# Optimization experiments

Hardware: AMD Instinct MI355X
Metric: run time of the kernel (lower is better)

Reference implementation:

```python
import jax, jax.numpy as jnp
import jax.scipy as jsp
import numpy as np

NUM_EMBEDDINGS = 256
EMBEDDING_DIM = 64
SPARSITY_LEVEL = 4
N_BINS = 16
COEF_MAX = 3.0
COEF_MU = 50.0
COMMITMENT_COST = 0.25
EPSILON = 1e-10


def _normalize_dict(dictionary):
    # F.normalize(dict, p=2, dim=0, eps): x / max(||x||_2, eps) per column
    nrm = jnp.linalg.norm(dictionary, axis=0, keepdims=True)
    return dictionary / jnp.maximum(nrm, EPSILON)


def _quantize_coeff_mu_law(coeff):
    inv_log1p_mu = 1.0 / np.log1p(COEF_MU)  # scalar constant
    c = jnp.clip(coeff, -COEF_MAX, COEF_MAX) / COEF_MAX
    encoded = jnp.sign(c) * jnp.log1p(jnp.abs(c) * COEF_MU) * inv_log1p_mu
    scaled = (encoded + 1.0) * ((N_BINS - 1) / 2.0)
    bin_idx = jnp.clip(jnp.round(scaled).astype(jnp.int32), 0, N_BINS - 1)
    # dequantize
    z = bin_idx.astype(coeff.dtype) * (2.0 / (N_BINS - 1)) - 1.0
    decoded = jnp.sign(z) * (jnp.expm1(jnp.abs(z) / inv_log1p_mu) / COEF_MU) * COEF_MAX
    return bin_idx, decoded


def batch_omp_with_support(X, Dn, K):
    # X: [M, Bs] signals, Dn: [M, N] normalized dictionary
    G = Dn.T @ Dn                       # [N, N] Gram
    h_bar = (Dn.T @ X).T                # [Bs, N] correlations
    Bs, N = h_bar.shape
    dt = h_bar.dtype
    h = h_bar
    mask = jnp.zeros((Bs, N), dtype=bool)
    L = jnp.ones((Bs, 1, 1), dtype=dt)  # incremental Cholesky of G[I, I]
    I = jnp.zeros((Bs, 0), dtype=jnp.int32)
    x_sel = jnp.zeros((Bs, 0), dtype=dt)
    rows = jnp.arange(Bs)
    for k in range(1, K + 1):  # K is small & static -> unrolled
        idx = jnp.argmax(jnp.abs(h) * (~mask), axis=1).astype(jnp.int32)
        mask = mask.at[rows, idx].set(True)
        if k > 1:
            G_stack = G[I, idx[:, None]]                     # [Bs, k-1]
            w = jsp.linalg.solve_triangular(L, G_stack[..., None], lower=True)  # [Bs,k-1,1]
            wT = jnp.swapaxes(w, 1, 2)                       # [Bs,1,k-1]
            w_corner = jnp.sqrt(jnp.clip(1.0 - jnp.sum(wT * wT, axis=2, keepdims=True), 1e-12))
            top = jnp.concatenate([L, jnp.zeros((Bs, k - 1, 1), dt)], axis=2)
            bot = jnp.concatenate([wT, w_corner], axis=2)
            L = jnp.concatenate([top, bot], axis=1)          # [Bs,k,k]
        I = jnp.concatenate([I, idx[:, None]], axis=1)       # [Bs,k]
        h_stack = jnp.take_along_axis(h_bar, I, axis=1)[..., None]  # [Bs,k,1]
        # cholesky_solve: L L^T x = h
        y = jsp.linalg.solve_triangular(L, h_stack, lower=True)
        xs = jsp.linalg.solve_triangular(jnp.swapaxes(L, 1, 2), y, lower=False)
        x_sel = xs[..., 0]                                   # [Bs,k] coeffs aligned w/ support
        beta = jnp.einsum('bk,bkn->bn', x_sel, G[I])         # [Bs,N]
        h = h_bar - beta
    return I, x_sel


def setup_inputs() -> dict:
    key = jax.random.key(0)
    k1, k2 = jax.random.split(key)
    z_e = jax.random.normal(k1, (32, EMBEDDING_DIM, 64, 64), dtype=jnp.float32)
    dictionary = jax.random.normal(k2, (EMBEDDING_DIM, NUM_EMBEDDINGS), dtype=jnp.float32) * 0.02
    return {"z_e": z_e, "dictionary": dictionary}


def reference(z_e, dictionary):
    B, C, H, W = z_e.shape
    Dn = _normalize_dict(dictionary)
    signals = jnp.transpose(z_e, (0, 2, 3, 1)).reshape(-1, C).T  # [C, B*H*W]
    # OMP runs with no grad (torch.no_grad in original)
    support, coeffs = jax.lax.stop_gradient(
        batch_omp_with_support(jax.lax.stop_gradient(signals), jax.lax.stop_gradient(Dn), SPARSITY_LEVEL)
    )
    # mu-law quantize coefficients (constants w.r.t. grads)
    bin_idx, coeffs_q = _quantize_coeff_mu_law(coeffs)
    # reconstruct with quantized coeffs; dictionary path is differentiable
    atoms = Dn.T[support]                                    # [Bs, K, C]
    recon_flat = jnp.einsum('bkc,bk->bc', atoms, coeffs_q)
    recon = jnp.transpose(recon_flat.reshape(B, H, W, C), (0, 3, 1, 2))
    # VQ-VAE style losses + STE
    e_latent_loss = jnp.mean((jax.lax.stop_gradient(recon) - z_e) ** 2)
    q_latent_loss = jnp.mean((recon - jax.lax.stop_gradient(z_e)) ** 2)
    loss = q_latent_loss + COMMITMENT_COST * e_latent_loss
    z_q = z_e + jax.lax.stop_gradient(recon - z_e)
    return z_q, loss


if __name__ == '__main__':
    out = reference(**setup_inputs())
    print(out[0].shape, out[1])
```

## Files before the change

### kernel.cpp

```cpp
#include <hip/hip_runtime.h>
#include <math.h>

#define NEMB 256
#define DIM 64
#define SIGS 128
#define THREADS 512
#define NSIG 131072
#define GRID (NSIG / SIGS)

#define LOG1P50 3.9318256327243257
#define INV_MU_F ((float)(1.0 / LOG1P50))
#define TWO15_F ((float)(2.0 / 15.0))

#define LB_SIG   0
#define LB_XS    32768
#define LB_QI    34816
#define LB_RED   36864
#define LDS_BYTES 36928

#define DPP_MAX(v, ctrl, rmask)  do {                                          \
    int _vi = __float_as_int(v);                                               \
    int _ti = __builtin_amdgcn_update_dpp(_vi, _vi, (ctrl), (rmask), 0xf, false);\
    (v) = fmaxf((v), __int_as_float(_ti));                                     \
} while (0)

__global__ void k_normalize(const float* __restrict__ D, float* __restrict__ Dn)
{
#pragma clang fp contract(off)
    int n = threadIdx.x;
    float ss = 0.0f;
    for (int c = 0; c < DIM; c++) {
        float v = D[c * NEMB + n];
        float sq = v * v;
        ss = ss + sq;
    }
    float nrm = fmaxf(sqrtf(ss), 1e-10f);
    for (int c = 0; c < DIM; c++)
        Dn[c * NEMB + n] = D[c * NEMB + n] / nrm;
}

__global__ void k_gram(const float* __restrict__ Dn, float* __restrict__ G)
{
    __shared__ float coli[DIM];
    int i = blockIdx.x, j = threadIdx.x;
    if (j < DIM) coli[j] = Dn[j * NEMB + i];
    __syncthreads();
    float s = 0.0f;
#pragma unroll
    for (int c = 0; c < DIM; c++) s = fmaf(coli[c], Dn[c * NEMB + j], s);
    G[i * NEMB + j] = s;
}

__device__ __forceinline__ float quant_decode(float coeff)
{
#pragma clang fp contract(off)
    float c = fminf(fmaxf(coeff, -3.0f), 3.0f) / 3.0f;
    float ac = fabsf(c);
    float sgn = (c > 0.0f) ? 1.0f : ((c < 0.0f) ? -1.0f : 0.0f);
    float l = log1pf(ac * 50.0f);
    float enc = (sgn * l) * INV_MU_F;
    float scaled = (enc + 1.0f) * 7.5f;
    int bin = (int)rintf(scaled);
    bin = bin < 0 ? 0 : (bin > 15 ? 15 : bin);
    float t = (float)bin * TWO15_F;
    float zv = t - 1.0f;
    float az = fabsf(zv);
    float sz = (zv > 0.0f) ? 1.0f : ((zv < 0.0f) ? -1.0f : 0.0f);
    float e = expm1f(az / INV_MU_F);
    return (sz * (e / 50.0f)) * 3.0f;
}

__device__ __forceinline__ void omp_signal(const float* hb4, int lane,
                                           const float* __restrict__ G,
                                           float* __restrict__ xsv,
                                           int* __restrict__ qi, int s)
{
#pragma clang fp contract(off)
    float hbsi[4] = {hb4[0], hb4[1], hb4[2], hb4[3]};
    float h[4] = {hbsi[0], hbsi[1], hbsi[2], hbsi[3]};
    float Lm[4][4];
    float Gr[3][4];
    int Iv[4];
    float hsel[4];
    float xs[4];
    float y[4];
    int m4 = 0;
#pragma unroll
    for (int kk = 0; kk < 4; kk++) {
        float bv = -1.0f;
        int bj = 0;
#pragma unroll
        for (int j = 0; j < 4; j++) {
            float v = (m4 & (1 << j)) ? 0.0f : fabsf(h[j]);
            if (v > bv) { bv = v; bj = j; }
        }
        float red = bv;
        DPP_MAX(red, 0x111, 0xf);
        DPP_MAX(red, 0x112, 0xf);
        DPP_MAX(red, 0x114, 0xf);
        DPP_MAX(red, 0x118, 0xf);
        DPP_MAX(red, 0x142, 0xa);
        DPP_MAX(red, 0x143, 0xc);
        float vmax = __int_as_float(__builtin_amdgcn_readlane(__float_as_int(red), 63));
        unsigned long long mball = __ballot(bv == vmax);
        int owner = __ffsll(mball) - 1;
        int idx = __builtin_amdgcn_readlane(4 * lane + bj, owner);
        if (lane == owner) m4 |= (1 << bj);
        if (kk < 3) {
            const float4 gt = *(const float4*)(G + (size_t)idx * NEMB + 4 * lane);
            Gr[kk][0] = gt.x; Gr[kk][1] = gt.y; Gr[kk][2] = gt.z; Gr[kk][3] = gt.w;
        }
        if (kk > 0) {
            float Gs[3], w[3];
#pragma unroll
            for (int j = 0; j < 3; j++)
                if (j < kk) Gs[j] = G[(size_t)Iv[j] * NEMB + idx];
#pragma unroll
            for (int r = 0; r < 3; r++) {
                if (r < kk) {
                    float acc = 0.0f;
#pragma unroll
                    for (int cc = 0; cc < 3; cc++)
                        if (cc < r) { float p = Lm[r][cc] * w[cc]; acc = acc + p; }
                    float t2 = Gs[r] - acc;
                    w[r] = t2 / Lm[r][r];
                }
            }
            float ssum = 0.0f;
#pragma unroll
            for (int j = 0; j < 3; j++)
                if (j < kk) { float p = w[j] * w[j]; ssum = ssum + p; }
            float om = 1.0f - ssum;
            float wc = sqrtf(fmaxf(om, 1e-12f));
#pragma unroll
            for (int cc = 0; cc < 3; cc++)
                if (cc < kk) Lm[kk][cc] = w[cc];
            Lm[kk][kk] = wc;
        } else {
            Lm[0][0] = 1.0f;
        }
        Iv[kk] = idx;
        {
            float hbsel = (bj == 0) ? hbsi[0] : ((bj == 1) ? hbsi[1] : ((bj == 2) ? hbsi[2] : hbsi[3]));
            hsel[kk] = __int_as_float(__builtin_amdgcn_readlane(__float_as_int(hbsel), owner));
        }
        {
            float acc = 0.0f;
#pragma unroll
            for (int cc = 0; cc < 3; cc++)
                if (cc < kk) { float p = Lm[kk][cc] * y[cc]; acc = acc + p; }
            float t2 = hsel[kk] - acc;
            y[kk] = t2 / Lm[kk][kk];
        }
#pragma unroll
        for (int r = 3; r >= 0; r--) {
            if (r <= kk) {
                float acc = 0.0f;
#pragma unroll
                for (int cc = 0; cc < 4; cc++)
                    if (cc > r && cc <= kk) { float p = Lm[cc][r] * xs[cc]; acc = acc + p; }
                float t2 = y[r] - acc;
                xs[r] = t2 / Lm[r][r];
            }
        }
        if (kk < 3) {
#pragma unroll
            for (int j = 0; j < 4; j++) {
                float bsum = 0.0f;
#pragma unroll
                for (int jj = 0; jj < 3; jj++)
                    if (jj <= kk) { float p = xs[jj] * Gr[jj][j]; bsum = bsum + p; }
                h[j] = hbsi[j] - bsum;
            }
        }
    }
    if (lane == 0) {
#pragma unroll
        for (int j = 0; j < 4; j++) {
            xsv[j * SIGS + s] = xs[j];
            qi[j * SIGS + s] = Iv[j];
        }
    }
}

__launch_bounds__(THREADS, 8)
__global__ void k_omp(const float* __restrict__ z,
                      const float* __restrict__ Dn_g,
                      const float* __restrict__ G,
                      double* __restrict__ loss_acc,
                      float* __restrict__ zq)
{
    extern __shared__ char smem[];
    float* sig = (float*)(smem + LB_SIG);
    float* xsv = (float*)(smem + LB_XS);
    int* qi = (int*)(smem + LB_QI);
    double* red = (double*)(smem + LB_RED);

    int tid = threadIdx.x;
    int lane = tid & 63;
    int wid = tid >> 6;

    long sbase = (long)blockIdx.x * SIGS;
    int b = (int)(sbase >> 12);
    int pl0 = (int)(sbase & 4095);
    const float* zb = z + ((size_t)b << 18) + pl0;
    {
        int w = tid & (SIGS - 1);
        int g = tid >> 7;
#pragma unroll
        for (int i = 0; i < 16; i++) {
            int c = g * 16 + i;
            sig[c * SIGS + w] = zb[(size_t)c * 4096 + w];
        }
    }
    __syncthreads();

    for (int g2 = 0; g2 < 2; g2++) {
        int s0 = wid * 16 + g2 * 8;
        float hb[8][4];
#pragma unroll
        for (int a = 0; a < 8; a++)
#pragma unroll
            for (int t = 0; t < 4; t++) hb[a][t] = 0.0f;
#pragma unroll 8
        for (int c = 0; c < DIM; c++) {
            float4 sva = *(const float4*)(sig + c * SIGS + s0);
            float4 svb = *(const float4*)(sig + c * SIGS + s0 + 4);
            float s8[8] = {sva.x, sva.y, sva.z, sva.w, svb.x, svb.y, svb.z, svb.w};
            float4 dv = *(const float4*)(Dn_g + c * NEMB + 4 * lane);
            float d4[4] = {dv.x, dv.y, dv.z, dv.w};
#pragma unroll
            for (int a = 0; a < 8; a++) {
                hb[a][0] = fmaf(s8[a], d4[0], hb[a][0]);
                hb[a][1] = fmaf(s8[a], d4[1], hb[a][1]);
                hb[a][2] = fmaf(s8[a], d4[2], hb[a][2]);
                hb[a][3] = fmaf(s8[a], d4[3], hb[a][3]);
            }
        }
#pragma unroll
        for (int a = 0; a < 8; a++)
            omp_signal(hb[a], lane, G, xsv, qi, s0 + a);
    }
    __syncthreads();

    {
        int jq = tid >> 7;
        int wq = tid & (SIGS - 1);
        xsv[jq * SIGS + wq] = quant_decode(xsv[jq * SIGS + wq]);
    }
    __syncthreads();

    double lsum = 0.0;
    float* zqb = zq + ((size_t)b << 18) + pl0;
    {
#pragma clang fp contract(off)
        int w = tid & (SIGS - 1);
        int g = tid >> 7;
        float q0 = xsv[0 * SIGS + w], q1 = xsv[1 * SIGS + w];
        float q2 = xsv[2 * SIGS + w], q3 = xsv[3 * SIGS + w];
        int i0 = qi[0 * SIGS + w], i1 = qi[1 * SIGS + w];
        int i2 = qi[2 * SIGS + w], i3 = qi[3 * SIGS + w];
#pragma unroll
        for (int ci = 0; ci < 16; ci++) {
            int c = g * 16 + ci;
            const float* dr = Dn_g + c * NEMB;
            float p0 = q0 * dr[i0];
            float p1 = q1 * dr[i1];
            float p2 = q2 * dr[i2];
            float p3 = q3 * dr[i3];
            float r = p0 + p1;
            r = r + p2;
            r = r + p3;
            float zev = sig[c * SIGS + w];
            float d = r - zev;
            float zqv = zev + d;
            lsum += (double)d * (double)d;
            zqb[(size_t)c * 4096 + w] = zqv;
        }
    }
#pragma unroll
    for (int off = 32; off > 0; off >>= 1) lsum += __shfl_xor(lsum, off);
    if (lane == 0) red[wid] = lsum;
    __syncthreads();
    if (tid == 0) {
        double t = 0.0;
#pragma unroll
        for (int i = 0; i < 8; i++) t += red[i];
        atomicAdd(loss_acc, t);
    }
}

__global__ void k_final(const double* __restrict__ loss_acc, float* __restrict__ out)
{
    double m = loss_acc[0] / 8388608.0;
    out[0] = (float)(m + 0.25 * m);
}

extern "C" void kernel_launch(void* const* d_in, const int* in_sizes, int n_in,
                              void* d_out, int out_size, void* d_ws, size_t ws_size,
                              hipStream_t stream)
{
    const float* z = (const float*)d_in[0];
    const float* D = (const float*)d_in[1];
    float* out = (float*)d_out;
    char* ws = (char*)d_ws;
    double* loss_acc = (double*)ws;
    float* Dn = (float*)(ws + 256);
    float* G = (float*)(ws + 256 + 65536);

    hipMemsetAsync(loss_acc, 0, sizeof(double), stream);
    k_normalize<<<1, NEMB, 0, stream>>>(D, Dn);
    k_gram<<<NEMB, NEMB, 0, stream>>>(Dn, G);
    hipFuncSetAttribute(reinterpret_cast<const void*>(k_omp),
                        hipFuncAttributeMaxDynamicSharedMemorySize, LDS_BYTES);
    k_omp<<<GRID, THREADS, LDS_BYTES, stream>>>(z, Dn, G, loss_acc, out);
    k_final<<<1, 1, 0, stream>>>(loss_acc, out + 8388608);
    (void)in_sizes; (void)n_in; (void)out_size; (void)ws_size;
}
```

Before: 315.8 us.

## Interleave OMP across eight signals per wave, distributing Cholesky work to lanes

The per-signal OMP loop is restructured so the eight signals a wave handles advance through each sparsity step together. The small Cholesky and triangular solves now run once, with lane a holding signal a's state, instead of being repeated redundantly by all lanes for each signal in turn. Residuals are recomputed from stored support indices by reloading Gram rows, which trades extra G loads for fewer serial scalar chains and more independent work per step. Separately, launch bounds drop from 8 to 6 to allow more registers, the loss memset is folded into k_normalize, and that kernel now stages D through LDS.

```diff
diff --git a/kernel.cpp b/kernel.cpp
--- a/kernel.cpp
+++ b/kernel.cpp
@@ -24,19 +24,30 @@
     (v) = fmaxf((v), __int_as_float(_ti));                                     \
 } while (0)
 
-__global__ void k_normalize(const float* __restrict__ D, float* __restrict__ Dn)
+static __device__ __forceinline__ float rl_f(float v, int lane)
+{ return __int_as_float(__builtin_amdgcn_readlane(__float_as_int(v), lane)); }
+
+__global__ void k_normalize(const float* __restrict__ D, float* __restrict__ Dn,
+                            double* __restrict__ loss_acc)
 {
 #pragma clang fp contract(off)
-    int n = threadIdx.x;
+    extern __shared__ float ds[];
+    int tid = threadIdx.x;
+    const float4* s4 = (const float4*)D;
+    float4* d4 = (float4*)ds;
+#pragma unroll
+    for (int i = 0; i < 16; i++) d4[i * 256 + tid] = s4[i * 256 + tid];
+    if (tid == 0) *loss_acc = 0.0;
+    __syncthreads();
     float ss = 0.0f;
     for (int c = 0; c < DIM; c++) {
-        float v = D[c * NEMB + n];
+        float v = ds[c * NEMB + tid];
         float sq = v * v;
         ss = ss + sq;
     }
     float nrm = fmaxf(sqrtf(ss), 1e-10f);
     for (int c = 0; c < DIM; c++)
-        Dn[c * NEMB + n] = D[c * NEMB + n] / nrm;
+        Dn[c * NEMB + tid] = ds[c * NEMB + tid] / nrm;
 }
 
 __global__ void k_gram(const float* __restrict__ Dn, float* __restrict__ G)
@@ -70,120 +81,7 @@
     return (sz * (e / 50.0f)) * 3.0f;
 }
 
-__device__ __forceinline__ void omp_signal(const float* hb4, int lane,
-                                           const float* __restrict__ G,
-                                           float* __restrict__ xsv,
-                                           int* __restrict__ qi, int s)
-{
-#pragma clang fp contract(off)
-    float hbsi[4] = {hb4[0], hb4[1], hb4[2], hb4[3]};
-    float h[4] = {hbsi[0], hbsi[1], hbsi[2], hbsi[3]};
-    float Lm[4][4];
-    float Gr[3][4];
-    int Iv[4];
-    float hsel[4];
-    float xs[4];
-    float y[4];
-    int m4 = 0;
-#pragma unroll
-    for (int kk = 0; kk < 4; kk++) {
-        float bv = -1.0f;
-        int bj = 0;
-#pragma unroll
-        for (int j = 0; j < 4; j++) {
-            float v = (m4 & (1 << j)) ? 0.0f : fabsf(h[j]);
-            if (v > bv) { bv = v; bj = j; }
-        }
-        float red = bv;
-        DPP_MAX(red, 0x111, 0xf);
-        DPP_MAX(red, 0x112, 0xf);
-        DPP_MAX(red, 0x114, 0xf);
-        DPP_MAX(red, 0x118, 0xf);
-        DPP_MAX(red, 0x142, 0xa);
-        DPP_MAX(red, 0x143, 0xc);
-        float vmax = __int_as_float(__builtin_amdgcn_readlane(__float_as_int(red), 63));
-        unsigned long long mball = __ballot(bv == vmax);
-        int owner = __ffsll(mball) - 1;
-        int idx = __builtin_amdgcn_readlane(4 * lane + bj, owner);
-        if (lane == owner) m4 |= (1 << bj);
-        if (kk < 3) {
-            const float4 gt = *(const float4*)(G + (size_t)idx * NEMB + 4 * lane);
-            Gr[kk][0] = gt.x; Gr[kk][1] = gt.y; Gr[kk][2] = gt.z; Gr[kk][3] = gt.w;
-        }
-        if (kk > 0) {
-            float Gs[3], w[3];
-#pragma unroll
-            for (int j = 0; j < 3; j++)
-                if (j < kk) Gs[j] = G[(size_t)Iv[j] * NEMB + idx];
-#pragma unroll
-            for (int r = 0; r < 3; r++) {
-                if (r < kk) {
-                    float acc = 0.0f;
-#pragma unroll
-                    for (int cc = 0; cc < 3; cc++)
-                        if (cc < r) { float p = Lm[r][cc] * w[cc]; acc = acc + p; }
-                    float t2 = Gs[r] - acc;
-                    w[r] = t2 / Lm[r][r];
-                }
-            }
-            float ssum = 0.0f;
-#pragma unroll
-            for (int j = 0; j < 3; j++)
-                if (j < kk) { float p = w[j] * w[j]; ssum = ssum + p; }
-            float om = 1.0f - ssum;
-            float wc = sqrtf(fmaxf(om, 1e-12f));
-#pragma unroll
-            for (int cc = 0; cc < 3; cc++)
-                if (cc < kk) Lm[kk][cc] = w[cc];
-            Lm[kk][kk] = wc;
-        } else {
-            Lm[0][0] = 1.0f;
-        }
-        Iv[kk] = idx;
-        {
-            float hbsel = (bj == 0) ? hbsi[0] : ((bj == 1) ? hbsi[1] : ((bj == 2) ? hbsi[2] : hbsi[3]));
-            hsel[kk] = __int_as_float(__builtin_amdgcn_readlane(__float_as_int(hbsel), owner));
-        }
-        {
-            float acc = 0.0f;
-#pragma unroll
-            for (int cc = 0; cc < 3; cc++)
-                if (cc < kk) { float p = Lm[kk][cc] * y[cc]; acc = acc + p; }
-            float t2 = hsel[kk] - acc;
-            y[kk] = t2 / Lm[kk][kk];
-        }
-#pragma unroll
-        for (int r = 3; r >= 0; r--) {
-            if (r <= kk) {
-                float acc = 0.0f;
-#pragma unroll
-                for (int cc = 0; cc < 4; cc++)
-                    if (cc > r && cc <= kk) { float p = Lm[cc][r] * xs[cc]; acc = acc + p; }
-                float t2 = y[r] - acc;
-                xs[r] = t2 / Lm[r][r];
-            }
-        }
-        if (kk < 3) {
-#pragma unroll
-            for (int j = 0; j < 4; j++) {
-                float bsum = 0.0f;
-#pragma unroll
-                for (int jj = 0; jj < 3; jj++)
-                    if (jj <= kk) { float p = xs[jj] * Gr[jj][j]; bsum = bsum + p; }
-                h[j] = hbsi[j] - bsum;
-            }
-        }
-    }
-    if (lane == 0) {
-#pragma unroll
-        for (int j = 0; j < 4; j++) {
-            xsv[j * SIGS + s] = xs[j];
-            qi[j * SIGS + s] = Iv[j];
-        }
-    }
-}
-
-__launch_bounds__(THREADS, 8)
+__launch_bounds__(THREADS, 6)
 __global__ void k_omp(const float* __restrict__ z,
                       const float* __restrict__ Dn_g,
                       const float* __restrict__ G,
@@ -237,9 +135,133 @@
                 hb[a][3] = fmaf(s8[a], d4[3], hb[a][3]);
             }
         }
-#pragma unroll
-        for (int a = 0; a < 8; a++)
-            omp_signal(hb[a], lane, G, xsv, qi, s0 + a);
+
+        {
+#pragma clang fp contract(off)
+            unsigned m4 = 0;
+            float Lm[4][4];
+            float y[4], xs[4];
+            int vIv[4] = {0, 0, 0, 0};
+            int vidx = 0;
+            float vhsel = 0.0f;
+            int IvS[8][4];
+            Lm[0][0] = 1.0f; Lm[1][1] = 1.0f; Lm[2][2] = 1.0f; Lm[3][3] = 1.0f;
+
+#pragma unroll
+            for (int kk = 0; kk < 4; kk++) {
+                float sxs[3][8];
+                if (kk > 0) {
+#pragma unroll
+                    for (int a = 0; a < 8; a++)
+#pragma unroll
+                        for (int jj = 0; jj < 3; jj++)
+                            if (jj < kk) sxs[jj][a] = rl_f(xs[jj], a);
+                }
+#pragma unroll
+                for (int a = 0; a < 8; a++) {
+                    float h[4];
+                    if (kk == 0) {
+                        h[0] = hb[a][0]; h[1] = hb[a][1]; h[2] = hb[a][2]; h[3] = hb[a][3];
+                    } else {
+                        float gr[3][4];
+#pragma unroll
+                        for (int jj = 0; jj < 3; jj++)
+                            if (jj < kk) {
+                                const float4 gv = *(const float4*)(G + (size_t)IvS[a][jj] * NEMB + 4 * lane);
+                                gr[jj][0] = gv.x; gr[jj][1] = gv.y; gr[jj][2] = gv.z; gr[jj][3] = gv.w;
+                            }
+#pragma unroll
+                        for (int j = 0; j < 4; j++) {
+                            float bsum = 0.0f;
+#pragma unroll
+                            for (int jj = 0; jj < 3; jj++)
+                                if (jj < kk) { float p = sxs[jj][a] * gr[jj][j]; bsum = bsum + p; }
+                            h[j] = hb[a][j] - bsum;
+                        }
+                    }
+                    float bv = -1.0f;
+                    int bj = 0;
+#pragma unroll
+                    for (int j = 0; j < 4; j++) {
+                        float v = (m4 & (1u << (4 * a + j))) ? 0.0f : fabsf(h[j]);
+                        if (v > bv) { bv = v; bj = j; }
+                    }
+                    float rd = bv;
+                    DPP_MAX(rd, 0x111, 0xf);
+                    DPP_MAX(rd, 0x112, 0xf);
+                    DPP_MAX(rd, 0x114, 0xf);
+                    DPP_MAX(rd, 0x118, 0xf);
+                    DPP_MAX(rd, 0x142, 0xa);
+                    DPP_MAX(rd, 0x143, 0xc);
+                    float vmax = rl_f(rd, 63);
+                    unsigned long long mball = __ballot(bv == vmax);
+                    int owner = __ffsll(mball) - 1;
+                    int idx = __builtin_amdgcn_readlane(4 * lane + bj, owner);
+                    if (lane == owner) m4 |= (1u << (4 * a + bj));
+                    float hbsel = (bj == 0) ? hb[a][0] : ((bj == 1) ? hb[a][1] : ((bj == 2) ? hb[a][2] : hb[a][3]));
+                    float hs = rl_f(hbsel, owner);
+                    bool isa = (lane == a);
+                    vidx = isa ? idx : vidx;
+                    vhsel = isa ? hs : vhsel;
+                    vIv[kk] = isa ? idx : vIv[kk];
+                    IvS[a][kk] = idx;
+                }
+                if (kk > 0) {
+                    float Gs[3], w[3];
+#pragma unroll
+                    for (int jj = 0; jj < 3; jj++)
+                        if (jj < kk) Gs[jj] = G[(unsigned)(vIv[jj] * NEMB + vidx)];
+#pragma unroll
+                    for (int r = 0; r < 3; r++) {
+                        if (r < kk) {
+                            float acc = 0.0f;
+#pragma unroll
+                            for (int cc = 0; cc < 3; cc++)
+                                if (cc < r) { float p = Lm[r][cc] * w[cc]; acc = acc + p; }
+                            float t2 = Gs[r] - acc;
+                            w[r] = t2 / Lm[r][r];
+                        }
+                    }
+                    float ssum = 0.0f;
+#pragma unroll
+                    for (int jj = 0; jj < 3; jj++)
+                        if (jj < kk) { float p = w[jj] * w[jj]; ssum = ssum + p; }
+                    float om = 1.0f - ssum;
+                    float wc = sqrtf(fmaxf(om, 1e-12f));
+#pragma unroll
+                    for (int cc = 0; cc < 3; cc++)
+                        if (cc < kk) Lm[kk][cc] = w[cc];
+                    Lm[kk][kk] = wc;
+                }
+                {
+                    float acc = 0.0f;
+#pragma unroll
+                    for (int cc = 0; cc < 3; cc++)
+                        if (cc < kk) { float p = Lm[kk][cc] * y[cc]; acc = acc + p; }
+                    float t2 = vhsel - acc;
+                    y[kk] = t2 / Lm[kk][kk];
+                }
+#pragma unroll
+                for (int r = 3; r >= 0; r--) {
+                    if (r <= kk) {
+                        float acc = 0.0f;
+#pragma unroll
+                        for (int cc = 0; cc < 4; cc++)
+                            if (cc > r && cc <= kk) { float p = Lm[cc][r] * xs[cc]; acc = acc + p; }
+                        float t2 = y[r] - acc;
+                        xs[r] = t2 / Lm[r][r];
+                    }
+                }
+            }
+            if (lane < 8) {
+                int s = s0 + lane;
+#pragma unroll
+                for (int j = 0; j < 4; j++) {
+                    xsv[j * SIGS + s] = xs[j];
+                    qi[j * SIGS + s] = vIv[j];
+                }
+            }
+        }
     }
     __syncthreads();
 
@@ -308,11 +330,12 @@
     float* Dn = (float*)(ws + 256);
     float* G = (float*)(ws + 256 + 65536);
 
-    hipMemsetAsync(loss_acc, 0, sizeof(double), stream);
-    k_normalize<<<1, NEMB, 0, stream>>>(D, Dn);
+    (void)hipFuncSetAttribute(reinterpret_cast<const void*>(k_normalize),
+                              hipFuncAttributeMaxDynamicSharedMemorySize, 65536);
+    k_normalize<<<1, NEMB, 65536, stream>>>(D, Dn, loss_acc);
     k_gram<<<NEMB, NEMB, 0, stream>>>(Dn, G);
-    hipFuncSetAttribute(reinterpret_cast<const void*>(k_omp),
-                        hipFuncAttributeMaxDynamicSharedMemorySize, LDS_BYTES);
+    (void)hipFuncSetAttribute(reinterpret_cast<const void*>(k_omp),
+                              hipFuncAttributeMaxDynamicSharedMemorySize, LDS_BYTES);
     k_omp<<<GRID, THREADS, LDS_BYTES, stream>>>(z, Dn, G, loss_acc, out);
     k_final<<<1, 1, 0, stream>>>(loss_acc, out + 8388608);
     (void)in_sizes; (void)n_in; (void)out_size; (void)ws_size;
```

New measurement: 304.7 us. 1.04x faster.
